# Kernel optimization log

Measured on AMD Instinct MI355X. Metric: run time of the kernel, lower is better.

Reference implementation:

```python
import jax, jax.numpy as jnp
import numpy as np

P, B, A, NT = 2, 96, 32, 24
N = B * A
MD, MA, MW = 4, 4, 2
NPOLB = MD + MA
C_LK = 0.089793561062583294  # 1 / (2 * pi**1.5)


def _norm(v):
    return v / jnp.sqrt(jnp.sum(v * v, -1, keepdims=True) + 1e-12)


def _gat_atoms(c, i):
    # c: [P,B,A,3], i: [P,B,K] -> [P,B,K,3]
    return jnp.take_along_axis(c, jnp.broadcast_to(i[..., None], i.shape + (3,)), axis=2)


def setup_inputs():
    key = jax.random.key(0)
    rng = np.random.default_rng(0)
    inp = {}
    inp["pose_coords"] = jax.random.normal(key, (P, N, 3), jnp.float32) * 8.0
    inp["pose_stack_block_type"] = jnp.asarray(rng.integers(0, NT, (P, B)), jnp.int32)
    inp["pose_stack_min_bond_separation"] = jnp.full((P, B, B), 6, jnp.int32)
    inp["bt_n_atoms"] = jnp.full((NT,), A, jnp.int32)
    bonds = np.stack([np.arange(A), (np.arange(A) + 1) % A], -1)
    inp["bt_all_bonds"] = jnp.asarray(np.broadcast_to(bonds, (NT, A, 2)).copy(), jnp.int32)
    rngs = np.stack([np.arange(A), np.arange(A) + 1], -1)
    inp["bt_atom_all_bond_ranges"] = jnp.asarray(np.broadcast_to(rngs, (NT, A, 2)).copy(), jnp.int32)
    inp["bt_tile_n_donH"] = jnp.asarray(rng.integers(1, MD + 1, (NT,)), jnp.int32)
    inp["bt_tile_n_acc"] = jnp.asarray(rng.integers(1, MA + 1, (NT,)), jnp.int32)
    donH = np.broadcast_to(2 * np.arange(MD) + 1, (NT, MD)).copy()
    inp["bt_tile_donH_inds"] = jnp.asarray(donH, jnp.int32)
    inp["bt_tile_don_hvy_inds"] = jnp.asarray(donH - 1, jnp.int32)
    inp["bt_tile_acc_inds"] = jnp.asarray(np.broadcast_to(8 + np.arange(MA), (NT, MA)).copy(), jnp.int32)
    inp["bt_tile_hybridization"] = jnp.asarray(rng.integers(0, 3, (NT, MA)), jnp.int32)
    is_h = np.zeros((NT, A), np.int32)
    is_h[:, 1:8:2] = 1
    inp["bt_atom_is_hydrogen"] = jnp.asarray(is_h)
    par = np.empty((NT, A, 4), np.float32)
    par[..., 0] = rng.uniform(1.4, 2.2, (NT, A))   # lj_radius
    par[..., 1] = rng.uniform(-6.0, 6.0, (NT, A))  # lk_dgfree
    par[..., 2] = rng.uniform(3.0, 3.6, (NT, A))   # lk_lambda
    par[..., 3] = rng.uniform(3.0, 15.0, (NT, A))  # lk_volume
    inp["bt_tile_lk_ball_params"] = jnp.asarray(par)
    pd = np.minimum(np.abs(np.arange(A)[:, None] - np.arange(A)[None, :]), 6)
    inp["bt_path_distance"] = jnp.asarray(np.broadcast_to(pd, (NT, A, A)).copy(), jnp.int32)
    inp["lk_ball_global_params"] = jnp.asarray([6.0, 3.709, 2.828], jnp.float32)   # cutoff, ramp_width_A2, d2_low
    inp["water_gen_global_params"] = jnp.asarray([2.65, 2.0943951], jnp.float32)   # water dist, water bond angle
    inp["sp2_water_tors"] = jnp.asarray([0.0, np.pi], jnp.float32)
    inp["sp3_water_tors"] = jnp.asarray([np.pi / 3.0, -np.pi / 3.0], jnp.float32)
    inp["ring_water_tors"] = jnp.asarray([0.0, np.pi / 2.0], jnp.float32)
    return inp


def reference(pose_coords, pose_stack_block_type, pose_stack_min_bond_separation,
              bt_n_atoms, bt_all_bonds, bt_atom_all_bond_ranges,
              bt_tile_n_donH, bt_tile_n_acc, bt_tile_donH_inds, bt_tile_don_hvy_inds,
              bt_tile_acc_inds, bt_tile_hybridization, bt_atom_is_hydrogen,
              bt_tile_lk_ball_params, bt_path_distance,
              lk_ball_global_params, water_gen_global_params,
              sp2_water_tors, sp3_water_tors, ring_water_tors):
    bt = pose_stack_block_type
    coords = pose_coords.reshape(P, B, A, 3)
    wdist = water_gen_global_params[0]
    wang = water_gen_global_params[1]
    # ---- step 1a: donor waters placed along heavy->H direction ----
    hvy_i = bt_tile_don_hvy_inds[bt]
    H_i = bt_tile_donH_inds[bt]                                              # [P,B,MD]
    hvy = _gat_atoms(coords, hvy_i)
    Hxyz = _gat_atoms(coords, H_i)
    don_w = hvy + wdist * _norm(Hxyz - hvy)                                  # [P,B,MD,3]
    don_mask = jnp.arange(MD) < bt_tile_n_donH[bt][..., None]                # [P,B,MD]
    don_w = jnp.broadcast_to(don_w[..., None, :], (P, B, MD, MW, 3))
    don_wm = don_mask[..., None] & (jnp.arange(MW) == 0)                     # one water per donH
    # ---- step 1b: acceptor waters via hybridization-dependent torsion (NeRF) ----
    acc_i = bt_tile_acc_inds[bt]                                             # [P,B,MA]
    ranges0 = bt_atom_all_bond_ranges[bt][..., 0]                            # [P,B,A]
    bonds1 = bt_all_bonds[bt][..., 1]                                        # [P,B,A]
    base_i = jnp.take_along_axis(bonds1, jnp.take_along_axis(ranges0, acc_i, axis=2), axis=2)
    base2_i = jnp.take_along_axis(bonds1, jnp.take_along_axis(ranges0, base_i, axis=2), axis=2)
    cxyz = _gat_atoms(coords, acc_i)
    bxyz = _gat_atoms(coords, base_i)
    axyz = _gat_atoms(coords, base2_i)
    e1 = _norm(cxyz - bxyz)
    nrm = _norm(jnp.cross(bxyz - axyz, e1))
    e2 = jnp.cross(nrm, e1)
    tors_tab = jnp.stack([sp2_water_tors, sp3_water_tors, ring_water_tors])  # [3,MW]
    chi = tors_tab[bt_tile_hybridization[bt]]                                # [P,B,MA,MW]
    ct, st = jnp.cos(wang), jnp.sin(wang)
    acc_w = (cxyz[..., None, :]
             + (-wdist * ct) * e1[..., None, :]
             + (wdist * st) * jnp.cos(chi)[..., None] * e2[..., None, :]
             + (wdist * st) * jnp.sin(chi)[..., None] * nrm[..., None, :])   # [P,B,MA,MW,3]
    acc_mask = jnp.arange(MA) < bt_tile_n_acc[bt][..., None]
    acc_wm = jnp.broadcast_to(acc_mask[..., None], (P, B, MA, MW))
    # ---- assemble polar sites + waters ----
    waters = jnp.concatenate([don_w, acc_w], axis=2).reshape(P, B * NPOLB, MW, 3)
    wmask = jnp.concatenate([don_wm, acc_wm], axis=2).reshape(P, B * NPOLB, MW)
    pol_loc = jnp.concatenate([hvy_i, acc_i], axis=2)                        # [P,B,NPOLB]
    pol_mask = jnp.concatenate([don_mask, acc_mask], axis=2).reshape(P, B * NPOLB)
    gidx = (jnp.arange(B)[None, :, None] * A + pol_loc).reshape(P, B * NPOLB)
    # ---- gather per-atom data ----
    params_flat = bt_tile_lk_ball_params[bt].reshape(P, N, 4)
    heavy = bt_atom_is_hydrogen[bt].reshape(P, N) == 0
    xp = jnp.take_along_axis(pose_coords, jnp.broadcast_to(gidx[..., None], gidx.shape + (3,)), axis=1)
    pp = jnp.take_along_axis(params_flat, jnp.broadcast_to(gidx[..., None], gidx.shape + (4,)), axis=1)
    # ---- step 2: pair distances + bond-separation mask ----
    diff = xp[:, :, None, :] - pose_coords[:, None, :, :]                    # [P,NPOL,N,3]
    d2 = jnp.maximum(jnp.sum(diff * diff, -1), 1e-2)
    d = jnp.sqrt(d2)
    b_i = gidx // A
    a_i = gidx % A
    b_j = jnp.arange(N) // A
    a_j = jnp.arange(N) % A
    bti = jnp.take_along_axis(bt, b_i, axis=1)
    intra = bt_path_distance[bti[:, :, None], a_i[:, :, None], a_j[None, None, :]]
    inter = pose_stack_min_bond_separation[jnp.arange(P)[:, None, None], b_i[:, :, None], b_j[None, None, :]]
    sep = jnp.where(b_i[:, :, None] == b_j[None, None, :], intra, inter)
    cutoff = lk_ball_global_params[0]
    ramp2 = lk_ball_global_params[1]
    d2_low = lk_ball_global_params[2]
    mask = (sep >= 4) & heavy[:, None, :] & pol_mask[:, :, None] & (d < cutoff)
    # ---- isotropic LK desolvation of polar atom i by occluder j ----
    ri, dgi, lami = pp[..., 0], pp[..., 1], pp[..., 2]
    rj, volj = params_flat[..., 0], params_flat[..., 3]
    x = (d - (ri[:, :, None] + rj[:, None, :])) / lami[:, :, None]
    lk_iso = C_LK * dgi[:, :, None] * volj[:, None, :] / lami[:, :, None] * jnp.exp(-x * x) / d2
    lk_iso = jnp.where(mask, lk_iso, 0.0)
    # ---- lk-ball fraction from water-site occlusion ----
    wdiff = waters[:, :, :, None, :] - pose_coords[:, None, None, :, :]      # [P,NPOL,MW,N,3]
    d2w = jnp.sum(wdiff * wdiff, -1)
    d2w = jnp.where(wmask[..., None], d2w, 1e9)
    d2wmin = jnp.min(d2w, axis=2)                                            # [P,NPOL,N]
    wt = jnp.clip((d2_low + ramp2 - d2wmin) / ramp2, 0.0, 1.0)
    frac = wt * wt * (3.0 - 2.0 * wt)
    return jnp.stack([jnp.sum(lk_iso, (1, 2)), jnp.sum(lk_iso * frac, (1, 2))])  # [2,P]
```

## Files before the change

kernel.cpp:

```cpp
#include <hip/hip_runtime.h>
#include <math.h>

constexpr int P  = 2;
constexpr int B  = 96;
constexpr int A  = 32;
constexpr int NT = 24;
constexpr int N  = B * A;
constexpr int MD = 4;
constexpr int MA = 4;
constexpr int NPOL = MD + MA;
constexpr float C_LK = 0.0897935610625833f;

__global__ void zero_out_kernel(float* out) {
    int t = threadIdx.x;
    if (t < 2 * P) out[t] = 0.0f;
}

struct Polar {
    float xp[3];
    float ri, dgi, lami;
    float w0[3];
    float w1[3];
    int   wm0, wm1;
    int   valid;
    int   a_i;
    int   bti;
};

__global__ __launch_bounds__(256) void lkball_kernel(
    const float* __restrict__ pose_coords,
    const int*   __restrict__ block_type,
    const int*   __restrict__ min_sep,
    const int*   __restrict__ all_bonds,
    const int*   __restrict__ bond_ranges,
    const int*   __restrict__ n_donH,
    const int*   __restrict__ n_acc,
    const int*   __restrict__ donH_inds,
    const int*   __restrict__ don_hvy_inds,
    const int*   __restrict__ acc_inds,
    const int*   __restrict__ hyb,
    const int*   __restrict__ is_h,
    const float* __restrict__ lk_params,
    const int*   __restrict__ path_dist,
    const float* __restrict__ glob,
    const float* __restrict__ wglob,
    const float* __restrict__ sp2t,
    const float* __restrict__ sp3t,
    const float* __restrict__ ringt,
    float*       __restrict__ out)
{
    __shared__ Polar sp;
    __shared__ int   spath[A];
    __shared__ int   smsep[B];
    __shared__ float red0[4], red1[4];

    const int bid = blockIdx.x;
    const int p   = bid / (B * NPOL);
    const int rem = bid % (B * NPOL);
    const int b   = rem / NPOL;
    const int k   = rem % NPOL;
    const int tid = threadIdx.x;

    if (tid == 0) {
        const int bt = block_type[p * B + b];
        sp.bti = bt;
        const float wdist = wglob[0];
        const float wang  = wglob[1];

        if (k < MD) {
            const int nd  = n_donH[bt];
            sp.valid = (k < nd) ? 1 : 0;
            const int hvy = don_hvy_inds[bt * MD + k];
            const int Hi  = donH_inds[bt * MD + k];
            sp.a_i = hvy;
            const float* hc = pose_coords + (size_t)(p * N + b * A + hvy) * 3;
            const float* Hc = pose_coords + (size_t)(p * N + b * A + Hi) * 3;
            float dx = Hc[0] - hc[0], dy = Hc[1] - hc[1], dz = Hc[2] - hc[2];
            float inv = 1.0f / sqrtf(dx * dx + dy * dy + dz * dz + 1e-12f);
            sp.xp[0] = hc[0]; sp.xp[1] = hc[1]; sp.xp[2] = hc[2];
            sp.w0[0] = hc[0] + wdist * dx * inv;
            sp.w0[1] = hc[1] + wdist * dy * inv;
            sp.w0[2] = hc[2] + wdist * dz * inv;
            sp.w1[0] = 0.f; sp.w1[1] = 0.f; sp.w1[2] = 0.f;
            sp.wm0 = sp.valid;
            sp.wm1 = 0;
        } else {
            const int kk = k - MD;
            const int na = n_acc[bt];
            sp.valid = (kk < na) ? 1 : 0;
            const int ai = acc_inds[bt * MA + kk];
            sp.a_i = ai;
            const int r0    = bond_ranges[(bt * A + ai) * 2 + 0];
            const int base  = all_bonds[(bt * A + r0) * 2 + 1];
            const int r0b   = bond_ranges[(bt * A + base) * 2 + 0];
            const int base2 = all_bonds[(bt * A + r0b) * 2 + 1];
            const float* c  = pose_coords + (size_t)(p * N + b * A + ai)    * 3;
            const float* bx = pose_coords + (size_t)(p * N + b * A + base)  * 3;
            const float* ax = pose_coords + (size_t)(p * N + b * A + base2) * 3;

            float e1x = c[0] - bx[0], e1y = c[1] - bx[1], e1z = c[2] - bx[2];
            float inv1 = 1.0f / sqrtf(e1x * e1x + e1y * e1y + e1z * e1z + 1e-12f);
            e1x *= inv1; e1y *= inv1; e1z *= inv1;

            float ux = bx[0] - ax[0], uy = bx[1] - ax[1], uz = bx[2] - ax[2];
            float nx = uy * e1z - uz * e1y;
            float ny = uz * e1x - ux * e1z;
            float nz = ux * e1y - uy * e1x;
            float inv2 = 1.0f / sqrtf(nx * nx + ny * ny + nz * nz + 1e-12f);
            nx *= inv2; ny *= inv2; nz *= inv2;
            float e2x = ny * e1z - nz * e1y;
            float e2y = nz * e1x - nx * e1z;
            float e2z = nx * e1y - ny * e1x;

            const int hy = hyb[bt * MA + kk];
            const float* tab = (hy == 0) ? sp2t : ((hy == 1) ? sp3t : ringt);
            const float ct = cosf(wang), st = sinf(wang);

            float chi0 = tab[0], chi1 = tab[1];
            float c0 = cosf(chi0), s0c = sinf(chi0);
            float c1 = cosf(chi1), s1c = sinf(chi1);

            sp.w0[0] = c[0] - wdist * ct * e1x + wdist * st * c0 * e2x + wdist * st * s0c * nx;
            sp.w0[1] = c[1] - wdist * ct * e1y + wdist * st * c0 * e2y + wdist * st * s0c * ny;
            sp.w0[2] = c[2] - wdist * ct * e1z + wdist * st * c0 * e2z + wdist * st * s0c * nz;
            sp.w1[0] = c[0] - wdist * ct * e1x + wdist * st * c1 * e2x + wdist * st * s1c * nx;
            sp.w1[1] = c[1] - wdist * ct * e1y + wdist * st * c1 * e2y + wdist * st * s1c * ny;
            sp.w1[2] = c[2] - wdist * ct * e1z + wdist * st * c1 * e2z + wdist * st * s1c * nz;
            sp.wm0 = sp.valid;
            sp.wm1 = sp.valid;
            sp.xp[0] = c[0]; sp.xp[1] = c[1]; sp.xp[2] = c[2];
        }
        const float* pr = lk_params + (size_t)(bt * A + sp.a_i) * 4;
        sp.ri   = pr[0];
        sp.dgi  = pr[1];
        sp.lami = pr[2];
    }
    __syncthreads();

    if (!sp.valid) return;

    if (tid < A)  spath[tid] = path_dist[(sp.bti * A + sp.a_i) * A + tid];
    if (tid >= 64 && tid < 64 + B) smsep[tid - 64] = min_sep[(p * B + b) * B + (tid - 64)];
    __syncthreads();

    const float xpx = sp.xp[0], xpy = sp.xp[1], xpz = sp.xp[2];
    const float ri = sp.ri, dgi = sp.dgi;
    const float inv_lam = 1.0f / sp.lami;
    const float w0x = sp.w0[0], w0y = sp.w0[1], w0z = sp.w0[2];
    const float w1x = sp.w1[0], w1y = sp.w1[1], w1z = sp.w1[2];
    const int wm0 = sp.wm0, wm1 = sp.wm1;
    const float cutoff = glob[0], ramp2 = glob[1], d2_low = glob[2];
    const float inv_ramp2 = 1.0f / ramp2;
    const float pref = C_LK * dgi * inv_lam;

    float acc0 = 0.0f, acc1 = 0.0f;

    for (int j = tid; j < N; j += 256) {
        const int b_j = j >> 5;
        const int a_j = j & (A - 1);
        const float* cj = pose_coords + (size_t)(p * N + j) * 3;
        const float cjx = cj[0], cjy = cj[1], cjz = cj[2];

        const float dx = xpx - cjx, dy = xpy - cjy, dz = xpz - cjz;
        float d2 = dx * dx + dy * dy + dz * dz;
        d2 = fmaxf(d2, 0.01f);
        const float d = sqrtf(d2);

        const int sep = (b_j == b) ? spath[a_j] : smsep[b_j];
        if (sep < 4 || d >= cutoff) continue;

        const int bt_j = block_type[p * B + b_j];
        if (is_h[bt_j * A + a_j] != 0) continue;

        const float rj   = lk_params[(size_t)(bt_j * A + a_j) * 4 + 0];
        const float volj = lk_params[(size_t)(bt_j * A + a_j) * 4 + 3];

        const float x  = (d - (ri + rj)) * inv_lam;
        const float lk = pref * volj * __expf(-x * x) / d2;

        float d0x = w0x - cjx, d0y = w0y - cjy, d0z = w0z - cjz;
        float d1x = w1x - cjx, d1y = w1y - cjy, d1z = w1z - cjz;
        float d2w0 = wm0 ? (d0x * d0x + d0y * d0y + d0z * d0z) : 1e9f;
        float d2w1 = wm1 ? (d1x * d1x + d1y * d1y + d1z * d1z) : 1e9f;
        float d2wmin = fminf(d2w0, d2w1);
        float wt = (d2_low + ramp2 - d2wmin) * inv_ramp2;
        wt = fminf(fmaxf(wt, 0.0f), 1.0f);
        const float frac = wt * wt * (3.0f - 2.0f * wt);

        acc0 += lk;
        acc1 += lk * frac;
    }

    for (int off = 32; off > 0; off >>= 1) {
        acc0 += __shfl_down(acc0, off);
        acc1 += __shfl_down(acc1, off);
    }
    const int wave = tid >> 6;
    const int lane = tid & 63;
    if (lane == 0) { red0[wave] = acc0; red1[wave] = acc1; }
    __syncthreads();
    if (tid == 0) {
        float t0 = red0[0] + red0[1] + red0[2] + red0[3];
        float t1 = red1[0] + red1[1] + red1[2] + red1[3];
        atomicAdd(&out[p], t0);
        atomicAdd(&out[P + p], t1);
    }
}

extern "C" void kernel_launch(void* const* d_in, const int* in_sizes, int n_in,
                              void* d_out, int out_size, void* d_ws, size_t ws_size,
                              hipStream_t stream) {
    const float* pose_coords  = (const float*)d_in[0];
    const int*   block_type   = (const int*)  d_in[1];
    const int*   min_sep      = (const int*)  d_in[2];
    const int*   all_bonds    = (const int*)  d_in[4];
    const int*   bond_ranges  = (const int*)  d_in[5];
    const int*   n_donH       = (const int*)  d_in[6];
    const int*   n_acc        = (const int*)  d_in[7];
    const int*   donH_inds    = (const int*)  d_in[8];
    const int*   don_hvy_inds = (const int*)  d_in[9];
    const int*   acc_inds     = (const int*)  d_in[10];
    const int*   hyb          = (const int*)  d_in[11];
    const int*   is_h         = (const int*)  d_in[12];
    const float* lk_params    = (const float*)d_in[13];
    const int*   path_dist    = (const int*)  d_in[14];
    const float* glob         = (const float*)d_in[15];
    const float* wglob        = (const float*)d_in[16];
    const float* sp2t         = (const float*)d_in[17];
    const float* sp3t         = (const float*)d_in[18];
    const float* ringt        = (const float*)d_in[19];
    float* out = (float*)d_out;

    zero_out_kernel<<<1, 64, 0, stream>>>(out);

    const int nblocks = P * B * NPOL;
    lkball_kernel<<<nblocks, 256, 0, stream>>>(
        pose_coords, block_type, min_sep, all_bonds, bond_ranges,
        n_donH, n_acc, donH_inds, don_hvy_inds, acc_inds, hyb, is_h,
        lk_params, path_dist, glob, wglob, sp2t, sp3t, ringt, out);
}
```

Measured before the change: 126.3 us.

## Process all polar atoms of a block per CTA with register-cached occluders

Each workgroup now handles all eight polar atoms of one residue against half of the occluder atoms, instead of one polar atom against every atom. Each thread keeps its occluder coordinates and parameters in registers and reuses them across the eight polars. Branches are replaced by predication, and the math uses fast sqrt and reciprocal intrinsics. This removes repeated global loads and the serial per-block setup, at the cost of fewer workgroups (384 instead of 1536) and no early exit for invalid polars.

```diff
diff --git a/kernel.cpp b/kernel.cpp
--- a/kernel.cpp
+++ b/kernel.cpp
@@ -4,28 +4,19 @@
 constexpr int P  = 2;
 constexpr int B  = 96;
 constexpr int A  = 32;
-constexpr int NT = 24;
 constexpr int N  = B * A;
 constexpr int MD = 4;
 constexpr int MA = 4;
 constexpr int NPOL = MD + MA;
+constexpr int SJ = 2;
+constexpr int JS = N / SJ;
+constexpr int JPT = JS / 256;
 constexpr float C_LK = 0.0897935610625833f;
 
 __global__ void zero_out_kernel(float* out) {
     int t = threadIdx.x;
     if (t < 2 * P) out[t] = 0.0f;
 }
-
-struct Polar {
-    float xp[3];
-    float ri, dgi, lami;
-    float w0[3];
-    float w1[3];
-    int   wm0, wm1;
-    int   valid;
-    int   a_i;
-    int   bti;
-};
 
 __global__ __launch_bounds__(256) void lkball_kernel(
     const float* __restrict__ pose_coords,
@@ -49,47 +40,46 @@
     const float* __restrict__ ringt,
     float*       __restrict__ out)
 {
-    __shared__ Polar sp;
-    __shared__ int   spath[A];
+    __shared__ float spolar[NPOL][16];
+    __shared__ int   spolai[NPOL];
+    __shared__ int   s_bt[B];
     __shared__ int   smsep[B];
+    __shared__ int   spath[NPOL * A];
     __shared__ float red0[4], red1[4];
 
-    const int bid = blockIdx.x;
-    const int p   = bid / (B * NPOL);
-    const int rem = bid % (B * NPOL);
-    const int b   = rem / NPOL;
-    const int k   = rem % NPOL;
-    const int tid = threadIdx.x;
-
-    if (tid == 0) {
+    const int bid   = blockIdx.x;
+    const int p     = bid / (B * SJ);
+    const int rem   = bid % (B * SJ);
+    const int b     = rem / SJ;
+    const int slice = rem % SJ;
+    const int tid   = threadIdx.x;
+
+    if (tid < NPOL) {
+        const int k  = tid;
         const int bt = block_type[p * B + b];
-        sp.bti = bt;
         const float wdist = wglob[0];
         const float wang  = wglob[1];
-
+        float xp[3], w0[3], w1[3];
+        int   a_i, valid;
         if (k < MD) {
-            const int nd  = n_donH[bt];
-            sp.valid = (k < nd) ? 1 : 0;
+            valid = (k < n_donH[bt]) ? 1 : 0;
             const int hvy = don_hvy_inds[bt * MD + k];
             const int Hi  = donH_inds[bt * MD + k];
-            sp.a_i = hvy;
+            a_i = hvy;
             const float* hc = pose_coords + (size_t)(p * N + b * A + hvy) * 3;
             const float* Hc = pose_coords + (size_t)(p * N + b * A + Hi) * 3;
             float dx = Hc[0] - hc[0], dy = Hc[1] - hc[1], dz = Hc[2] - hc[2];
             float inv = 1.0f / sqrtf(dx * dx + dy * dy + dz * dz + 1e-12f);
-            sp.xp[0] = hc[0]; sp.xp[1] = hc[1]; sp.xp[2] = hc[2];
-            sp.w0[0] = hc[0] + wdist * dx * inv;
-            sp.w0[1] = hc[1] + wdist * dy * inv;
-            sp.w0[2] = hc[2] + wdist * dz * inv;
-            sp.w1[0] = 0.f; sp.w1[1] = 0.f; sp.w1[2] = 0.f;
-            sp.wm0 = sp.valid;
-            sp.wm1 = 0;
+            xp[0] = hc[0]; xp[1] = hc[1]; xp[2] = hc[2];
+            w0[0] = hc[0] + wdist * dx * inv;
+            w0[1] = hc[1] + wdist * dy * inv;
+            w0[2] = hc[2] + wdist * dz * inv;
+            w1[0] = hc[0] + 1.0e3f; w1[1] = hc[1] + 1.0e3f; w1[2] = hc[2] + 1.0e3f;
         } else {
             const int kk = k - MD;
-            const int na = n_acc[bt];
-            sp.valid = (kk < na) ? 1 : 0;
+            valid = (kk < n_acc[bt]) ? 1 : 0;
             const int ai = acc_inds[bt * MA + kk];
-            sp.a_i = ai;
+            a_i = ai;
             const int r0    = bond_ranges[(bt * A + ai) * 2 + 0];
             const int base  = all_bonds[(bt * A + r0) * 2 + 1];
             const int r0b   = bond_ranges[(bt * A + base) * 2 + 0];
@@ -115,80 +105,98 @@
             const int hy = hyb[bt * MA + kk];
             const float* tab = (hy == 0) ? sp2t : ((hy == 1) ? sp3t : ringt);
             const float ct = cosf(wang), st = sinf(wang);
-
-            float chi0 = tab[0], chi1 = tab[1];
-            float c0 = cosf(chi0), s0c = sinf(chi0);
-            float c1 = cosf(chi1), s1c = sinf(chi1);
-
-            sp.w0[0] = c[0] - wdist * ct * e1x + wdist * st * c0 * e2x + wdist * st * s0c * nx;
-            sp.w0[1] = c[1] - wdist * ct * e1y + wdist * st * c0 * e2y + wdist * st * s0c * ny;
-            sp.w0[2] = c[2] - wdist * ct * e1z + wdist * st * c0 * e2z + wdist * st * s0c * nz;
-            sp.w1[0] = c[0] - wdist * ct * e1x + wdist * st * c1 * e2x + wdist * st * s1c * nx;
-            sp.w1[1] = c[1] - wdist * ct * e1y + wdist * st * c1 * e2y + wdist * st * s1c * ny;
-            sp.w1[2] = c[2] - wdist * ct * e1z + wdist * st * c1 * e2z + wdist * st * s1c * nz;
-            sp.wm0 = sp.valid;
-            sp.wm1 = sp.valid;
-            sp.xp[0] = c[0]; sp.xp[1] = c[1]; sp.xp[2] = c[2];
+            float c0 = cosf(tab[0]), s0 = sinf(tab[0]);
+            float c1 = cosf(tab[1]), s1 = sinf(tab[1]);
+
+            xp[0] = c[0]; xp[1] = c[1]; xp[2] = c[2];
+            w0[0] = c[0] - wdist * ct * e1x + wdist * st * c0 * e2x + wdist * st * s0 * nx;
+            w0[1] = c[1] - wdist * ct * e1y + wdist * st * c0 * e2y + wdist * st * s0 * ny;
+            w0[2] = c[2] - wdist * ct * e1z + wdist * st * c0 * e2z + wdist * st * s0 * nz;
+            w1[0] = c[0] - wdist * ct * e1x + wdist * st * c1 * e2x + wdist * st * s1 * nx;
+            w1[1] = c[1] - wdist * ct * e1y + wdist * st * c1 * e2y + wdist * st * s1 * ny;
+            w1[2] = c[2] - wdist * ct * e1z + wdist * st * c1 * e2z + wdist * st * s1 * nz;
         }
-        const float* pr = lk_params + (size_t)(bt * A + sp.a_i) * 4;
-        sp.ri   = pr[0];
-        sp.dgi  = pr[1];
-        sp.lami = pr[2];
-    }
+        const float* pr = lk_params + (size_t)(bt * A + a_i) * 4;
+        const float lam = pr[2];
+        spolar[k][0] = xp[0]; spolar[k][1] = xp[1]; spolar[k][2] = xp[2];
+        spolar[k][3] = w0[0]; spolar[k][4] = w0[1]; spolar[k][5] = w0[2];
+        spolar[k][6] = w1[0]; spolar[k][7] = w1[1]; spolar[k][8] = w1[2];
+        spolar[k][9]  = pr[0];
+        spolar[k][10] = valid ? (C_LK * pr[1] / lam) : 0.0f;
+        spolar[k][11] = 1.0f / lam;
+        spolai[k] = a_i;
+    }
+    if (tid >= 64 && tid < 64 + B)   s_bt[tid - 64]   = block_type[p * B + (tid - 64)];
+    if (tid >= 160 && tid < 160 + B) smsep[tid - 160] = min_sep[(p * B + b) * B + (tid - 160)];
     __syncthreads();
 
-    if (!sp.valid) return;
-
-    if (tid < A)  spath[tid] = path_dist[(sp.bti * A + sp.a_i) * A + tid];
-    if (tid >= 64 && tid < 64 + B) smsep[tid - 64] = min_sep[(p * B + b) * B + (tid - 64)];
+    {
+        const int k  = tid >> 5;
+        const int aj = tid & 31;
+        const int bt = s_bt[b];
+        spath[tid] = path_dist[(bt * A + spolai[k]) * A + aj];
+    }
     __syncthreads();
 
-    const float xpx = sp.xp[0], xpy = sp.xp[1], xpz = sp.xp[2];
-    const float ri = sp.ri, dgi = sp.dgi;
-    const float inv_lam = 1.0f / sp.lami;
-    const float w0x = sp.w0[0], w0y = sp.w0[1], w0z = sp.w0[2];
-    const float w1x = sp.w1[0], w1y = sp.w1[1], w1z = sp.w1[2];
-    const int wm0 = sp.wm0, wm1 = sp.wm1;
-    const float cutoff = glob[0], ramp2 = glob[1], d2_low = glob[2];
-    const float inv_ramp2 = 1.0f / ramp2;
-    const float pref = C_LK * dgi * inv_lam;
+    const float cutoff = glob[0];
+    const float inv_ramp2 = 1.0f / glob[1];
+    const float c3 = glob[2] + glob[1];
+    const int a_j = tid & 31;
+    const int jbase = slice * JS + tid;
+
+    float cx[JPT], cy[JPT], cz[JPT], rj[JPT], ve[JPT];
+    float msep_f[JPT];
+    int   intra[JPT];
+#pragma unroll
+    for (int i = 0; i < JPT; ++i) {
+        const int j   = jbase + 256 * i;
+        const int b_j = j >> 5;
+        const float* cj = pose_coords + (size_t)(p * N + j) * 3;
+        cx[i] = cj[0]; cy[i] = cj[1]; cz[i] = cj[2];
+        const int bt_j = s_bt[b_j];
+        const int hv   = is_h[bt_j * A + a_j];
+        const float4 pj = *(const float4*)(lk_params + (size_t)(bt_j * A + a_j) * 4);
+        rj[i] = pj.x;
+        ve[i] = hv ? 0.0f : pj.w;
+        msep_f[i] = (float)smsep[b_j];
+        intra[i]  = (b_j == b);
+    }
 
     float acc0 = 0.0f, acc1 = 0.0f;
 
-    for (int j = tid; j < N; j += 256) {
-        const int b_j = j >> 5;
-        const int a_j = j & (A - 1);
-        const float* cj = pose_coords + (size_t)(p * N + j) * 3;
-        const float cjx = cj[0], cjy = cj[1], cjz = cj[2];
-
-        const float dx = xpx - cjx, dy = xpy - cjy, dz = xpz - cjz;
-        float d2 = dx * dx + dy * dy + dz * dz;
-        d2 = fmaxf(d2, 0.01f);
-        const float d = sqrtf(d2);
-
-        const int sep = (b_j == b) ? spath[a_j] : smsep[b_j];
-        if (sep < 4 || d >= cutoff) continue;
-
-        const int bt_j = block_type[p * B + b_j];
-        if (is_h[bt_j * A + a_j] != 0) continue;
-
-        const float rj   = lk_params[(size_t)(bt_j * A + a_j) * 4 + 0];
-        const float volj = lk_params[(size_t)(bt_j * A + a_j) * 4 + 3];
-
-        const float x  = (d - (ri + rj)) * inv_lam;
-        const float lk = pref * volj * __expf(-x * x) / d2;
-
-        float d0x = w0x - cjx, d0y = w0y - cjy, d0z = w0z - cjz;
-        float d1x = w1x - cjx, d1y = w1y - cjy, d1z = w1z - cjz;
-        float d2w0 = wm0 ? (d0x * d0x + d0y * d0y + d0z * d0z) : 1e9f;
-        float d2w1 = wm1 ? (d1x * d1x + d1y * d1y + d1z * d1z) : 1e9f;
-        float d2wmin = fminf(d2w0, d2w1);
-        float wt = (d2_low + ramp2 - d2wmin) * inv_ramp2;
-        wt = fminf(fmaxf(wt, 0.0f), 1.0f);
-        const float frac = wt * wt * (3.0f - 2.0f * wt);
-
-        acc0 += lk;
-        acc1 += lk * frac;
+#pragma unroll
+    for (int k = 0; k < NPOL; ++k) {
+        const float px = spolar[k][0], py = spolar[k][1], pz = spolar[k][2];
+        const float w0x = spolar[k][3], w0y = spolar[k][4], w0z = spolar[k][5];
+        const float w1x = spolar[k][6], w1y = spolar[k][7], w1z = spolar[k][8];
+        const float ri = spolar[k][9], pref = spolar[k][10], inv_lam = spolar[k][11];
+        const float path_k = (float)spath[k * A + a_j];
+
+#pragma unroll
+        for (int i = 0; i < JPT; ++i) {
+            const float dx = px - cx[i], dy = py - cy[i], dz = pz - cz[i];
+            float d2 = fmaf(dx, dx, fmaf(dy, dy, dz * dz));
+            d2 = fmaxf(d2, 0.01f);
+            const float d = __builtin_amdgcn_sqrtf(d2);
+            const float sep = intra[i] ? path_k : msep_f[i];
+            const bool ok = (sep >= 4.0f) & (d < cutoff);
+
+            const float x = (d - ri - rj[i]) * inv_lam;
+            float lk = pref * ve[i] * __expf(-x * x) * __builtin_amdgcn_rcpf(d2);
+            lk = ok ? lk : 0.0f;
+
+            const float d0x = w0x - cx[i], d0y = w0y - cy[i], d0z = w0z - cz[i];
+            const float d1x = w1x - cx[i], d1y = w1y - cy[i], d1z = w1z - cz[i];
+            const float d2w0 = fmaf(d0x, d0x, fmaf(d0y, d0y, d0z * d0z));
+            const float d2w1 = fmaf(d1x, d1x, fmaf(d1y, d1y, d1z * d1z));
+            const float d2wmin = fminf(d2w0, d2w1);
+            float wt = (c3 - d2wmin) * inv_ramp2;
+            wt = fminf(fmaxf(wt, 0.0f), 1.0f);
+            const float frac = wt * wt * (3.0f - 2.0f * wt);
+
+            acc0 += lk;
+            acc1 = fmaf(lk, frac, acc1);
+        }
     }
 
     for (int off = 32; off > 0; off >>= 1) {
@@ -200,10 +208,8 @@
     if (lane == 0) { red0[wave] = acc0; red1[wave] = acc1; }
     __syncthreads();
     if (tid == 0) {
-        float t0 = red0[0] + red0[1] + red0[2] + red0[3];
-        float t1 = red1[0] + red1[1] + red1[2] + red1[3];
-        atomicAdd(&out[p], t0);
-        atomicAdd(&out[P + p], t1);
+        atomicAdd(&out[p],     red0[0] + red0[1] + red0[2] + red0[3]);
+        atomicAdd(&out[P + p], red1[0] + red1[1] + red1[2] + red1[3]);
     }
 }
 
@@ -233,7 +239,7 @@
 
     zero_out_kernel<<<1, 64, 0, stream>>>(out);
 
-    const int nblocks = P * B * NPOL;
+    const int nblocks = P * B * SJ;
     lkball_kernel<<<nblocks, 256, 0, stream>>>(
         pose_coords, block_type, min_sep, all_bonds, bond_ranges,
         n_donH, n_acc, donH_inds, don_hvy_inds, acc_inds, hyb, is_h,
```

Result: faster. 109.8 us (-13.1%).
